# Kernel optimization log

Measured on AMD Instinct MI355X. Metric: run time of the kernel, lower is better.

## Reference

```python
import jax, jax.numpy as jnp
import numpy as np

TOP_K = 2
E = 8      # num_experts
D = 1024   # model dim
F = 2048   # expert hidden dim = int(2*3072/3), already a multiple of 256
B, S = 2, 1024


def setup_inputs() -> dict:
    key = jax.random.key(0)
    ks = jax.random.split(key, 8)
    sc = 0.02
    return {
        "x_bsD": jax.random.normal(ks[0], (B, S, D), dtype=jnp.float32),
        "router_DE": jax.random.normal(ks[1], (D, E), dtype=jnp.float32) * sc,
        "w_in_shared_FD": jax.random.normal(ks[2], (F, D), dtype=jnp.float32) * sc,
        "w_out_shared_DF": jax.random.normal(ks[3], (D, F), dtype=jnp.float32) * sc,
        "w_swiglu_FD": jax.random.normal(ks[4], (F, D), dtype=jnp.float32) * sc,
        "w_in_eDF": jax.random.normal(ks[5], (E, D, F), dtype=jnp.float32) * sc,
        "w_swiglu_eDF": jax.random.normal(ks[6], (E, D, F), dtype=jnp.float32) * sc,
        "w_out_eFD": jax.random.normal(ks[7], (E, F, D), dtype=jnp.float32) * sc,
    }


def reference(x_bsD, router_DE, w_in_shared_FD, w_out_shared_DF, w_swiglu_FD,
              w_in_eDF, w_swiglu_eDF, w_out_eFD):
    b, s, d = x_bsD.shape
    x_aD = x_bsD.reshape(-1, d)                      # [a, D]
    a = x_aD.shape[0]

    # Router (token choice): top-k per token, others masked to -inf
    scores_aE = x_aD @ router_DE                      # [a, E]
    topv_aK, topi_aK = jax.lax.top_k(scores_aE, TOP_K)
    masked_aE = jnp.full_like(scores_aE, -jnp.inf)
    masked_aE = masked_aE.at[jnp.arange(a)[:, None], topi_aK].set(topv_aK)
    # sigmoid(-inf) == 0 -> non-selected (expert, token) pairs contribute nothing
    gates_Ea = jax.nn.sigmoid(masked_aE.astype(jnp.float32)).astype(x_aD.dtype).T  # [E, a]

    # Dispatch: router_indices_EG == arange(a) per expert, so gather == broadcast
    routed_in_EaD = x_aD[None, :, :] * gates_Ea[:, :, None]   # [E, a, D]
    routed_in_EaD = jax.lax.stop_gradient(routed_in_EaD)      # matches .detach()

    # Per-expert bmm SwiGLU
    mid_EaF = jnp.einsum('ead,edf->eaf', routed_in_EaD, w_in_eDF)
    sw_EaF = jnp.einsum('ead,edf->eaf', routed_in_EaD, w_swiglu_eDF)
    h_EaF = jax.nn.silu(mid_EaF) * sw_EaF
    out_EaD = jnp.einsum('eaf,efd->ead', h_EaF, w_out_eFD)

    # Shared expert (computed under torch.no_grad in the original)
    shared_aF = jax.nn.silu(x_aD @ w_in_shared_FD.T) * (x_aD @ w_swiglu_FD.T)
    shared_out_aD = jax.lax.stop_gradient(shared_aF @ w_out_shared_DF.T)

    # Combine: scatter_add with per-expert arange indices == sum over experts
    out_aD = shared_out_aD + jnp.sum(out_EaD, axis=0)
    return out_aD.reshape(b, s, d)
```

## Files before the change

### kernel.cpp

```cpp
#include <hip/hip_runtime.h>
#include <hip/hip_bf16.h>

#define A_TOK 2048
#define DDIM 1024
#define FDIM 2048
#define NEXP 8
#define NE9 9
#define SLOTS_R (2 * A_TOK)
#define SLOTS_T (SLOTS_R + A_TOK)
#define NB1 (2 * FDIM)

typedef __attribute__((ext_vector_type(8))) short short8v;
typedef __attribute__((ext_vector_type(4))) float f32x4;
typedef __attribute__((ext_vector_type(4))) ushort ushort4v;

#define BARRIER() asm volatile("s_barrier" ::: "memory")
#define VMCNT(n) asm volatile("s_waitcnt vmcnt(" #n ")" ::: "memory")

__device__ __forceinline__ void lds16(const void* g, void* l) {
  __builtin_amdgcn_global_load_lds((const __attribute__((address_space(1))) void*)g,
                                   (__attribute__((address_space(3))) void*)l, 16, 0, 0);
}

__device__ __forceinline__ float sigmoidf_(float x) { return 1.f / (1.f + __expf(-x)); }
__device__ __forceinline__ ushort f2bf(float x) {
  __hip_bfloat16 b = __float2bfloat16(x);
  ushort u; __builtin_memcpy(&u, &b, 2); return u;
}
__device__ __forceinline__ float bf2f(ushort u) {
  union { unsigned int i; float f; } x; x.i = (unsigned int)u << 16; return x.f;
}

__global__ void k_trA(const float* __restrict__ w_in, const float* __restrict__ w_sw,
                      ushort* __restrict__ wt12) {
  int z = blockIdx.z; int e = z & 7; int which = z >> 3;
  const float* in = (which ? w_sw : w_in) + (size_t)e * DDIM * FDIM;
  ushort* outb = wt12 + (size_t)e * NB1 * DDIM;
  __shared__ ushort tile[64][68];
  int r0 = blockIdx.y * 64, c0 = blockIdx.x * 64;
  int tid = threadIdx.x;
  int rr = tid >> 4, cq = tid & 15;
#pragma unroll
  for (int i = 0; i < 4; i++) {
    int r = i * 16 + rr;
    float4 v = *(const float4*)(in + (size_t)(r0 + r) * FDIM + c0 + cq * 4);
    ushort4v o = {f2bf(v.x), f2bf(v.y), f2bf(v.z), f2bf(v.w)};
    *(ushort4v*)&tile[r][cq * 4] = o;
  }
  __syncthreads();
  int cc = tid >> 4, rq = tid & 15;
#pragma unroll
  for (int i = 0; i < 4; i++) {
    int c = i * 16 + cc;
    int f = c0 + c;
    int rp = ((f >> 5) << 6) + (which << 5) + (f & 31);
    ushort4v o = {tile[rq * 4 + 0][c], tile[rq * 4 + 1][c],
                  tile[rq * 4 + 2][c], tile[rq * 4 + 3][c]};
    *(ushort4v*)(outb + (size_t)rp * DDIM + r0 + rq * 4) = o;
  }
}

__global__ void k_trB(const float* __restrict__ in0, ushort* __restrict__ out0) {
  const float* in = in0 + (size_t)blockIdx.z * FDIM * DDIM;
  ushort* out = out0 + (size_t)blockIdx.z * DDIM * FDIM;
  __shared__ ushort tile[64][68];
  int r0 = blockIdx.y * 64, c0 = blockIdx.x * 64;
  int tid = threadIdx.x;
  int rr = tid >> 4, cq = tid & 15;
#pragma unroll
  for (int i = 0; i < 4; i++) {
    int r = i * 16 + rr;
    float4 v = *(const float4*)(in + (size_t)(r0 + r) * DDIM + c0 + cq * 4);
    ushort4v o = {f2bf(v.x), f2bf(v.y), f2bf(v.z), f2bf(v.w)};
    *(ushort4v*)&tile[r][cq * 4] = o;
  }
  __syncthreads();
  int cc = tid >> 4, rq = tid & 15;
#pragma unroll
  for (int i = 0; i < 4; i++) {
    int c = i * 16 + cc;
    ushort4v o = {tile[rq * 4 + 0][c], tile[rq * 4 + 1][c],
                  tile[rq * 4 + 2][c], tile[rq * 4 + 3][c]};
    *(ushort4v*)(out + (size_t)(c0 + c) * FDIM + r0 + rq * 4) = o;
  }
}

__global__ void k_cvt_sh(const float* __restrict__ w_in_sh, const float* __restrict__ w_sw_sh,
                         const float* __restrict__ w_out_sh, ushort* __restrict__ wt12_8,
                         ushort* __restrict__ wtout_8) {
  int z = blockIdx.y, row = blockIdx.x, tid = threadIdx.x;
  if (z < 2) {
    const float* in = (z ? w_sw_sh : w_in_sh) + (size_t)row * DDIM;
    int rp = ((row >> 5) << 6) + (z << 5) + (row & 31);
    ushort* outr = wt12_8 + (size_t)rp * DDIM;
    float4 v = ((const float4*)in)[tid];
    ushort4v o = {f2bf(v.x), f2bf(v.y), f2bf(v.z), f2bf(v.w)};
    ((ushort4v*)outr)[tid] = o;
  } else {
    if (row >= DDIM) return;
    const float* in = w_out_sh + (size_t)row * FDIM;
    ushort* outr = wtout_8 + (size_t)row * FDIM;
#pragma unroll
    for (int i = 0; i < 2; i++) {
      float4 v = ((const float4*)in)[tid + 256 * i];
      ushort4v o = {f2bf(v.x), f2bf(v.y), f2bf(v.z), f2bf(v.w)};
      ((ushort4v*)outr)[tid + 256 * i] = o;
    }
  }
}

__global__ void k_router(const float* __restrict__ x, const float* __restrict__ rw,
                         __hip_bfloat16* __restrict__ xbf, int* __restrict__ counts,
                         int* __restrict__ top_e, float* __restrict__ top_g) {
  int t = blockIdx.x * 4 + (threadIdx.x >> 6);
  int l = threadIdx.x & 63;
  const float* xr = x + (size_t)t * DDIM;
  float acc[NEXP];
#pragma unroll
  for (int e = 0; e < NEXP; e++) acc[e] = 0.f;
#pragma unroll
  for (int i = 0; i < 16; i++) {
    int d = i * 64 + l;
    float v = xr[d];
    xbf[(size_t)t * DDIM + d] = __float2bfloat16(v);
    const float* rr = rw + (size_t)d * NEXP;
#pragma unroll
    for (int e = 0; e < NEXP; e++) acc[e] += v * rr[e];
  }
#pragma unroll
  for (int e = 0; e < NEXP; e++) {
#pragma unroll
    for (int s = 32; s > 0; s >>= 1) acc[e] += __shfl_xor(acc[e], s);
  }
  if (l == 0) {
    float b1 = -1e30f, b2 = -1e30f;
    int i1 = 0, i2 = 0;
#pragma unroll
    for (int e = 0; e < NEXP; e++) {
      float v = acc[e];
      if (v > b1) { b2 = b1; i2 = i1; b1 = v; i1 = e; }
      else if (v > b2) { b2 = v; i2 = e; }
    }
    atomicAdd(&counts[i1], 1);
    atomicAdd(&counts[i2], 1);
    top_e[t * 2 + 0] = i1; top_e[t * 2 + 1] = i2;
    top_g[t * 2 + 0] = sigmoidf_(b1); top_g[t * 2 + 1] = sigmoidf_(b2);
  }
}

__global__ void k_scan(int* __restrict__ counts, int* __restrict__ offs,
                       int* __restrict__ cursor) {
  if (threadIdx.x == 0 && blockIdx.x == 0) {
    counts[NEXP] = A_TOK;
    int s = 0;
    for (int e = 0; e < NE9; e++) { offs[e] = s; s += counts[e]; cursor[e] = 0; }
  }
}

__global__ void k_dispatch(const float* __restrict__ x, const int* __restrict__ top_e,
                           const float* __restrict__ top_g, const int* __restrict__ offs,
                           int* __restrict__ cursor, int* __restrict__ slot_of,
                           __hip_bfloat16* __restrict__ y) {
  int t = blockIdx.x * 4 + (threadIdx.x >> 6);
  int l = threadIdx.x & 63;
  int e0 = top_e[t * 2 + 0], e1 = top_e[t * 2 + 1];
  float g0 = top_g[t * 2 + 0], g1 = top_g[t * 2 + 1];
  int s0 = 0, s1 = 0;
  if (l == 0) {
    s0 = offs[e0] + atomicAdd(&cursor[e0], 1);
    s1 = offs[e1] + atomicAdd(&cursor[e1], 1);
    slot_of[t * 2 + 0] = s0; slot_of[t * 2 + 1] = s1;
  }
  s0 = __shfl(s0, 0); s1 = __shfl(s1, 0);
  const float* xr = x + (size_t)t * DDIM;
#pragma unroll
  for (int i = 0; i < 16; i++) {
    int d = i * 64 + l;
    float v = xr[d];
    y[(size_t)s0 * DDIM + d] = __float2bfloat16(v * g0);
    y[(size_t)s1 * DDIM + d] = __float2bfloat16(v * g1);
  }
}

__global__ __launch_bounds__(256, 3) void k_mlp1(
    const ushort* __restrict__ Abase, const ushort* __restrict__ Bbase,
    ushort* __restrict__ Obase, const int* __restrict__ d_cnt,
    const int* __restrict__ d_off) {
  constexpr int K = DDIM, NT = DDIM / 32;
  constexpr int BUF = 16384;
  __shared__ __align__(16) char smem[3 * BUF];
  int e = blockIdx.z;
  int cnt = d_cnt[e];
  int m0 = blockIdx.y * 128;
  if (m0 >= cnt) return;
  int roff = d_off[e];
  int n0 = blockIdx.x * 128;
  const ushort* B = Bbase + (size_t)e * NB1 * DDIM;
  int tid = threadIdx.x, w = tid >> 6, l = tid & 63;
  int wm = w >> 1, wn = w & 1, lr = l & 15, kg = l >> 4;
  size_t arow0 = (size_t)roff + m0;

  int srow = tid >> 2;
  int sgg = (tid & 3) ^ ((tid >> 3) & 3);
  const ushort* pA0 = Abase + (arow0 + srow) * (size_t)K + sgg * 8;
  const ushort* pA1 = pA0 + (size_t)64 * K;
  const ushort* pB0 = B + ((size_t)n0 + srow) * K + sgg * 8;
  const ushort* pB1 = pB0 + (size_t)64 * K;
  int tls = tid * 16;

  int xorg = (kg ^ ((lr >> 1) & 3)) << 4;
  int offA[4], offB[4];
#pragma unroll
  for (int i = 0; i < 4; i++) {
    offA[i] = (wm * 64 + i * 16 + lr) * 64 + xorg;
    offB[i] = 8192 + (wn * 64 + i * 16 + lr) * 64 + xorg;
  }

  f32x4 acc[4][4];
#pragma unroll
  for (int i = 0; i < 4; i++)
#pragma unroll
    for (int j = 0; j < 4; j++) acc[i][j] = {0.f, 0.f, 0.f, 0.f};

#pragma unroll
  for (int pt = 0; pt < 2; ++pt) {
    char* bb = smem + pt * BUF;
    lds16(pA0, bb + tls);         pA0 += 32;
    lds16(pA1, bb + 4096 + tls);  pA1 += 32;
    lds16(pB0, bb + 8192 + tls);  pB0 += 32;
    lds16(pB1, bb + 12288 + tls); pB1 += 32;
  }
  VMCNT(4);
  BARRIER();

  char* b0 = smem;
  char* b1 = smem + BUF;
  char* b2 = smem + 2 * BUF;
  for (int t = 0; t < NT; ++t) {
    bool st = (t + 2) < NT;
    short8v af[4], bf[4];
#pragma unroll
    for (int mf = 0; mf < 4; mf++) af[mf] = *(const short8v*)(b0 + offA[mf]);
#pragma unroll
    for (int nf = 0; nf < 2; nf++) bf[nf] = *(const short8v*)(b0 + offB[nf]);
    if (st) {
      lds16(pA0, b2 + tls);
      lds16(pA1, b2 + 4096 + tls);
    }
    pA0 += 32; pA1 += 32;
    BARRIER();
    __builtin_amdgcn_s_setprio(1);
#pragma unroll
    for (int nf = 0; nf < 2; nf++)
#pragma unroll
      for (int mf = 0; mf < 4; mf++)
        acc[mf][nf] = __builtin_amdgcn_mfma_f32_16x16x32_bf16(af[mf], bf[nf], acc[mf][nf], 0, 0, 0);
    __builtin_amdgcn_s_setprio(0);
    BARRIER();
#pragma unroll
    for (int nf = 2; nf < 4; nf++) bf[nf] = *(const short8v*)(b0 + offB[nf]);
    if (st) {
      lds16(pB0, b2 + 8192 + tls);
      lds16(pB1, b2 + 12288 + tls);
    }
    pB0 += 32; pB1 += 32;
    BARRIER();
    __builtin_amdgcn_s_setprio(1);
#pragma unroll
    for (int nf = 2; nf < 4; nf++)
#pragma unroll
      for (int mf = 0; mf < 4; mf++)
        acc[mf][nf] = __builtin_amdgcn_mfma_f32_16x16x32_bf16(af[mf], bf[nf], acc[mf][nf], 0, 0, 0);
    __builtin_amdgcn_s_setprio(0);
    if (t < NT - 1) {
      if (st) { VMCNT(4); } else { VMCNT(0); }
      BARRIER();
    }
    char* tmp = b0; b0 = b1; b1 = b2; b2 = tmp;
  }

  int j = (n0 >> 6) + wn;
#pragma unroll
  for (int mf = 0; mf < 4; mf++)
#pragma unroll
    for (int nf = 0; nf < 2; nf++)
#pragma unroll
      for (int r = 0; r < 4; r++) {
        int row = m0 + wm * 64 + mf * 16 + kg * 4 + r;
        if (row < cnt) {
          float mid = acc[mf][nf][r];
          float sw = acc[mf][nf + 2][r];
          float hv = mid * sigmoidf_(mid) * sw;
          int col = j * 32 + nf * 16 + lr;
          Obase[((size_t)roff + row) * FDIM + col] = f2bf(hv);
        }
      }
}

__global__ __launch_bounds__(256, 3) void k_mlp2(
    const ushort* __restrict__ Abase, const ushort* __restrict__ Bbase,
    ushort* __restrict__ part, const int* __restrict__ d_cnt,
    const int* __restrict__ d_off) {
  constexpr int K = FDIM, NT = 1024 / 32;
  constexpr int BUF = 16384;
  __shared__ __align__(16) char smem[3 * BUF];
  int e = blockIdx.z;
  int cnt = d_cnt[e];
  int mt = blockIdx.y >> 1, kz = blockIdx.y & 1;
  int m0 = mt * 128;
  if (m0 >= cnt) return;
  int roff = d_off[e];
  int n0 = blockIdx.x * 128;
  int kbeg = kz * 1024;
  const ushort* B = Bbase + (size_t)e * DDIM * FDIM;
  int tid = threadIdx.x, w = tid >> 6, l = tid & 63;
  int wm = w >> 1, wn = w & 1, lr = l & 15, kg = l >> 4;
  size_t arow0 = (size_t)roff + m0;

  int srow = tid >> 2;
  int sgg = (tid & 3) ^ ((tid >> 3) & 3);
  const ushort* pA0 = Abase + (arow0 + srow) * (size_t)K + kbeg + sgg * 8;
  const ushort* pA1 = pA0 + (size_t)64 * K;
  const ushort* pB0 = B + ((size_t)n0 + srow) * K + kbeg + sgg * 8;
  const ushort* pB1 = pB0 + (size_t)64 * K;
  int tls = tid * 16;

  int xorg = (kg ^ ((lr >> 1) & 3)) << 4;
  int offA[4], offB[4];
#pragma unroll
  for (int i = 0; i < 4; i++) {
    offA[i] = (wm * 64 + i * 16 + lr) * 64 + xorg;
    offB[i] = 8192 + (wn * 64 + i * 16 + lr) * 64 + xorg;
  }

  f32x4 acc[4][4];
#pragma unroll
  for (int i = 0; i < 4; i++)
#pragma unroll
    for (int j = 0; j < 4; j++) acc[i][j] = {0.f, 0.f, 0.f, 0.f};

#pragma unroll
  for (int pt = 0; pt < 2; ++pt) {
    char* bb = smem + pt * BUF;
    lds16(pA0, bb + tls);         pA0 += 32;
    lds16(pA1, bb + 4096 + tls);  pA1 += 32;
    lds16(pB0, bb + 8192 + tls);  pB0 += 32;
    lds16(pB1, bb + 12288 + tls); pB1 += 32;
  }
  VMCNT(4);
  BARRIER();

  char* b0 = smem;
  char* b1 = smem + BUF;
  char* b2 = smem + 2 * BUF;
  for (int t = 0; t < NT; ++t) {
    bool st = (t + 2) < NT;
    short8v af[4], bf[4];
#pragma unroll
    for (int mf = 0; mf < 4; mf++) af[mf] = *(const short8v*)(b0 + offA[mf]);
#pragma unroll
    for (int nf = 0; nf < 2; nf++) bf[nf] = *(const short8v*)(b0 + offB[nf]);
    if (st) {
      lds16(pA0, b2 + tls);
      lds16(pA1, b2 + 4096 + tls);
    }
    pA0 += 32; pA1 += 32;
    BARRIER();
    __builtin_amdgcn_s_setprio(1);
#pragma unroll
    for (int nf = 0; nf < 2; nf++)
#pragma unroll
      for (int mf = 0; mf < 4; mf++)
        acc[mf][nf] = __builtin_amdgcn_mfma_f32_16x16x32_bf16(af[mf], bf[nf], acc[mf][nf], 0, 0, 0);
    __builtin_amdgcn_s_setprio(0);
    BARRIER();
#pragma unroll
    for (int nf = 2; nf < 4; nf++) bf[nf] = *(const short8v*)(b0 + offB[nf]);
    if (st) {
      lds16(pB0, b2 + 8192 + tls);
      lds16(pB1, b2 + 12288 + tls);
    }
    pB0 += 32; pB1 += 32;
    BARRIER();
    __builtin_amdgcn_s_setprio(1);
#pragma unroll
    for (int nf = 2; nf < 4; nf++)
#pragma unroll
      for (int mf = 0; mf < 4; mf++)
        acc[mf][nf] = __builtin_amdgcn_mfma_f32_16x16x32_bf16(af[mf], bf[nf], acc[mf][nf], 0, 0, 0);
    __builtin_amdgcn_s_setprio(0);
    if (t < NT - 1) {
      if (st) { VMCNT(4); } else { VMCNT(0); }
      BARRIER();
    }
    char* tmp = b0; b0 = b1; b1 = b2; b2 = tmp;
  }

  ushort* outp = part + (size_t)kz * SLOTS_T * DDIM;
#pragma unroll
  for (int mf = 0; mf < 4; mf++)
#pragma unroll
    for (int nf = 0; nf < 4; nf++)
#pragma unroll
      for (int r = 0; r < 4; r++) {
        int row = m0 + wm * 64 + mf * 16 + kg * 4 + r;
        if (row < cnt) {
          int col = n0 + wn * 64 + nf * 16 + lr;
          outp[((size_t)roff + row) * DDIM + col] = f2bf(acc[mf][nf][r]);
        }
      }
}

__global__ void k_combine(const ushort* __restrict__ part, const int* __restrict__ slot_of,
                          float* __restrict__ out) {
  int t = blockIdx.x, q = threadIdx.x;
  int rows[3];
  rows[0] = slot_of[t * 2 + 0];
  rows[1] = slot_of[t * 2 + 1];
  rows[2] = SLOTS_R + t;
  size_t P = (size_t)SLOTS_T * DDIM;
  float o[4] = {0.f, 0.f, 0.f, 0.f};
#pragma unroll
  for (int kz = 0; kz < 2; kz++)
#pragma unroll
    for (int i = 0; i < 3; i++) {
      ushort4v v = *(const ushort4v*)(part + kz * P + (size_t)rows[i] * DDIM + q * 4);
#pragma unroll
      for (int j = 0; j < 4; j++) o[j] += bf2f(v[j]);
    }
  float4 ov = {o[0], o[1], o[2], o[3]};
  ((float4*)out)[(size_t)t * (DDIM / 4) + q] = ov;
}

extern "C" void kernel_launch(void* const* d_in, const int* in_sizes, int n_in,
                              void* d_out, int out_size, void* d_ws, size_t ws_size,
                              hipStream_t stream) {
  (void)in_sizes; (void)n_in; (void)out_size; (void)ws_size;
  const float* x        = (const float*)d_in[0];
  const float* router   = (const float*)d_in[1];
  const float* w_in_sh  = (const float*)d_in[2];
  const float* w_out_sh = (const float*)d_in[3];
  const float* w_sw_sh  = (const float*)d_in[4];
  const float* w_in_e   = (const float*)d_in[5];
  const float* w_sw_e   = (const float*)d_in[6];
  const float* w_out_e  = (const float*)d_in[7];
  float* out = (float*)d_out;

  char* ws = (char*)d_ws;
  size_t off = 0;
  auto alloc = [&](size_t bytes) -> char* {
    char* p = ws + off;
    off += (bytes + 255) & ~(size_t)255;
    return p;
  };
  ushort* wt12     = (ushort*)alloc((size_t)NE9 * NB1 * DDIM * 2);
  ushort* wt_out_t = (ushort*)alloc((size_t)NE9 * DDIM * FDIM * 2);
  __hip_bfloat16* y_all = (__hip_bfloat16*)alloc((size_t)SLOTS_R * DDIM * 2);
  __hip_bfloat16* xbf   = (__hip_bfloat16*)alloc((size_t)A_TOK * DDIM * 2);
  ushort* h        = (ushort*)alloc((size_t)SLOTS_T * FDIM * 2);
  int*   counts  = (int*)alloc(64);
  int*   offs    = (int*)alloc(64);
  int*   cursor  = (int*)alloc(64);
  int*   top_e   = (int*)alloc((size_t)A_TOK * 2 * 4);
  float* top_g   = (float*)alloc((size_t)A_TOK * 2 * 4);
  int*   slot_of = (int*)alloc((size_t)A_TOK * 2 * 4);
  (void)alloc(1 << 20);
  ushort* part = wt12;

  hipMemsetAsync(counts, 0, 64, stream);

  k_trA<<<dim3(FDIM / 64, DDIM / 64, 16), 256, 0, stream>>>(w_in_e, w_sw_e, wt12);
  k_trB<<<dim3(DDIM / 64, FDIM / 64, NEXP), 256, 0, stream>>>(w_out_e, wt_out_t);
  k_cvt_sh<<<dim3(FDIM, 3), 256, 0, stream>>>(
      w_in_sh, w_sw_sh, w_out_sh,
      wt12 + (size_t)NEXP * NB1 * DDIM, wt_out_t + (size_t)NEXP * DDIM * FDIM);

  k_router<<<dim3(A_TOK / 4), 256, 0, stream>>>(x, router, xbf, counts, top_e, top_g);
  k_scan<<<1, 64, 0, stream>>>(counts, offs, cursor);
  k_dispatch<<<dim3(A_TOK / 4), 256, 0, stream>>>(x, top_e, top_g, offs, cursor, slot_of, y_all);

  k_mlp1<<<dim3(NB1 / 128, A_TOK / 128, NE9), 256, 0, stream>>>(
      (const ushort*)y_all, wt12, h, counts, offs);

  k_mlp2<<<dim3(DDIM / 128, (A_TOK / 128) * 2, NE9), 256, 0, stream>>>(
      h, wt_out_t, part, counts, offs);

  k_combine<<<dim3(A_TOK), 256, 0, stream>>>(part, slot_of, out);
}
```

Before: 305.0 us.

## Fuse weight-prep kernels, fold scan into router, remap GEMM grids across XCDs

Merges the three weight conversion/transposition kernels and the counts memset into a single prep kernel, and folds the expert-offset scan into the router with a last-block ticket. This removes several kernel launches and a memset. The MLP GEMM grids are flattened to 1D and remapped so consecutive workgroups, which land on different XCDs, are spread across experts and tiles. That remap is meant to improve L2 locality and load balance. The ticket pattern relies on threadfence ordering for correctness.

```diff
diff --git a/kernel.cpp b/kernel.cpp
--- a/kernel.cpp
+++ b/kernel.cpp
@@ -10,6 +10,12 @@
 #define SLOTS_T (SLOTS_R + A_TOK)
 #define NB1 (2 * FDIM)
 
+#define PREP_TRA_END 8192
+#define PREP_TRB_END (PREP_TRA_END + 4096)
+#define PREP_SH12_END (PREP_TRB_END + 1024)
+#define PREP_SHOUT_END (PREP_SH12_END + 512)
+#define PREP_NWG (PREP_SHOUT_END + 1)
+
 typedef __attribute__((ext_vector_type(8))) short short8v;
 typedef __attribute__((ext_vector_type(4))) float f32x4;
 typedef __attribute__((ext_vector_type(4))) ushort ushort4v;
@@ -31,87 +37,100 @@
   union { unsigned int i; float f; } x; x.i = (unsigned int)u << 16; return x.f;
 }
 
-__global__ void k_trA(const float* __restrict__ w_in, const float* __restrict__ w_sw,
-                      ushort* __restrict__ wt12) {
-  int z = blockIdx.z; int e = z & 7; int which = z >> 3;
-  const float* in = (which ? w_sw : w_in) + (size_t)e * DDIM * FDIM;
-  ushort* outb = wt12 + (size_t)e * NB1 * DDIM;
+__global__ void k_prep(const float* __restrict__ w_in_e, const float* __restrict__ w_sw_e,
+                       const float* __restrict__ w_out_e, const float* __restrict__ w_in_sh,
+                       const float* __restrict__ w_sw_sh, const float* __restrict__ w_out_sh,
+                       ushort* __restrict__ wt12, ushort* __restrict__ wt_out_t,
+                       int* __restrict__ counts, int* __restrict__ ticket) {
   __shared__ ushort tile[64][68];
-  int r0 = blockIdx.y * 64, c0 = blockIdx.x * 64;
-  int tid = threadIdx.x;
-  int rr = tid >> 4, cq = tid & 15;
-#pragma unroll
-  for (int i = 0; i < 4; i++) {
-    int r = i * 16 + rr;
-    float4 v = *(const float4*)(in + (size_t)(r0 + r) * FDIM + c0 + cq * 4);
-    ushort4v o = {f2bf(v.x), f2bf(v.y), f2bf(v.z), f2bf(v.w)};
-    *(ushort4v*)&tile[r][cq * 4] = o;
-  }
-  __syncthreads();
-  int cc = tid >> 4, rq = tid & 15;
-#pragma unroll
-  for (int i = 0; i < 4; i++) {
-    int c = i * 16 + cc;
-    int f = c0 + c;
+  int b = blockIdx.x, tid = threadIdx.x;
+  if (b < PREP_TRA_END) {
+    int z = b >> 9, t2 = b & 511;
+    int e = z & 7, which = z >> 3;
+    const float* in = (which ? w_sw_e : w_in_e) + (size_t)e * DDIM * FDIM;
+    ushort* outb = wt12 + (size_t)e * NB1 * DDIM;
+    int c0 = (t2 & 31) * 64, r0 = (t2 >> 5) * 64;
+    int rr = tid >> 4, cq = tid & 15;
+#pragma unroll
+    for (int i = 0; i < 4; i++) {
+      int r = i * 16 + rr;
+      float4 v = *(const float4*)(in + (size_t)(r0 + r) * FDIM + c0 + cq * 4);
+      ushort4v o = {f2bf(v.x), f2bf(v.y), f2bf(v.z), f2bf(v.w)};
+      *(ushort4v*)&tile[r][cq * 4] = o;
+    }
+    __syncthreads();
+    int cc = tid >> 4, rq = tid & 15;
+#pragma unroll
+    for (int i = 0; i < 4; i++) {
+      int c = i * 16 + cc;
+      int f = c0 + c;
+      int rp = ((f >> 5) << 6) + (which << 5) + (f & 31);
+      ushort4v o = {tile[rq * 4 + 0][c], tile[rq * 4 + 1][c],
+                    tile[rq * 4 + 2][c], tile[rq * 4 + 3][c]};
+      *(ushort4v*)(outb + (size_t)rp * DDIM + r0 + rq * 4) = o;
+    }
+  } else if (b < PREP_TRB_END) {
+    int b2 = b - PREP_TRA_END;
+    int z = b2 >> 9, t2 = b2 & 511;
+    const float* in = w_out_e + (size_t)z * FDIM * DDIM;
+    ushort* out = wt_out_t + (size_t)z * DDIM * FDIM;
+    int c0 = (t2 & 15) * 64, r0 = (t2 >> 4) * 64;
+    int rr = tid >> 4, cq = tid & 15;
+#pragma unroll
+    for (int i = 0; i < 4; i++) {
+      int r = i * 16 + rr;
+      float4 v = *(const float4*)(in + (size_t)(r0 + r) * DDIM + c0 + cq * 4);
+      ushort4v o = {f2bf(v.x), f2bf(v.y), f2bf(v.z), f2bf(v.w)};
+      *(ushort4v*)&tile[r][cq * 4] = o;
+    }
+    __syncthreads();
+    int cc = tid >> 4, rq = tid & 15;
+#pragma unroll
+    for (int i = 0; i < 4; i++) {
+      int c = i * 16 + cc;
+      ushort4v o = {tile[rq * 4 + 0][c], tile[rq * 4 + 1][c],
+                    tile[rq * 4 + 2][c], tile[rq * 4 + 3][c]};
+      *(ushort4v*)(out + (size_t)(c0 + c) * FDIM + r0 + rq * 4) = o;
+    }
+  } else if (b < PREP_SH12_END) {
+    int j = b - PREP_TRB_END;
+    int rj = j * 4 + (tid >> 6);
+    int l = tid & 63;
+    int which = rj & 1, f = rj >> 1;
+    const float* src = (which ? w_sw_sh : w_in_sh) + (size_t)f * DDIM;
     int rp = ((f >> 5) << 6) + (which << 5) + (f & 31);
-    ushort4v o = {tile[rq * 4 + 0][c], tile[rq * 4 + 1][c],
-                  tile[rq * 4 + 2][c], tile[rq * 4 + 3][c]};
-    *(ushort4v*)(outb + (size_t)rp * DDIM + r0 + rq * 4) = o;
-  }
-}
-
-__global__ void k_trB(const float* __restrict__ in0, ushort* __restrict__ out0) {
-  const float* in = in0 + (size_t)blockIdx.z * FDIM * DDIM;
-  ushort* out = out0 + (size_t)blockIdx.z * DDIM * FDIM;
-  __shared__ ushort tile[64][68];
-  int r0 = blockIdx.y * 64, c0 = blockIdx.x * 64;
-  int tid = threadIdx.x;
-  int rr = tid >> 4, cq = tid & 15;
-#pragma unroll
-  for (int i = 0; i < 4; i++) {
-    int r = i * 16 + rr;
-    float4 v = *(const float4*)(in + (size_t)(r0 + r) * DDIM + c0 + cq * 4);
-    ushort4v o = {f2bf(v.x), f2bf(v.y), f2bf(v.z), f2bf(v.w)};
-    *(ushort4v*)&tile[r][cq * 4] = o;
-  }
-  __syncthreads();
-  int cc = tid >> 4, rq = tid & 15;
-#pragma unroll
-  for (int i = 0; i < 4; i++) {
-    int c = i * 16 + cc;
-    ushort4v o = {tile[rq * 4 + 0][c], tile[rq * 4 + 1][c],
-                  tile[rq * 4 + 2][c], tile[rq * 4 + 3][c]};
-    *(ushort4v*)(out + (size_t)(c0 + c) * FDIM + r0 + rq * 4) = o;
-  }
-}
-
-__global__ void k_cvt_sh(const float* __restrict__ w_in_sh, const float* __restrict__ w_sw_sh,
-                         const float* __restrict__ w_out_sh, ushort* __restrict__ wt12_8,
-                         ushort* __restrict__ wtout_8) {
-  int z = blockIdx.y, row = blockIdx.x, tid = threadIdx.x;
-  if (z < 2) {
-    const float* in = (z ? w_sw_sh : w_in_sh) + (size_t)row * DDIM;
-    int rp = ((row >> 5) << 6) + (z << 5) + (row & 31);
-    ushort* outr = wt12_8 + (size_t)rp * DDIM;
-    float4 v = ((const float4*)in)[tid];
-    ushort4v o = {f2bf(v.x), f2bf(v.y), f2bf(v.z), f2bf(v.w)};
-    ((ushort4v*)outr)[tid] = o;
+    ushort* dst = wt12 + (size_t)NEXP * NB1 * DDIM + (size_t)rp * DDIM;
+#pragma unroll
+    for (int i = 0; i < 4; i++) {
+      int q = l + 64 * i;
+      float4 v = ((const float4*)src)[q];
+      ushort4v o = {f2bf(v.x), f2bf(v.y), f2bf(v.z), f2bf(v.w)};
+      ((ushort4v*)dst)[q] = o;
+    }
+  } else if (b < PREP_SHOUT_END) {
+    int j = b - PREP_SH12_END;
+    int d = j * 2 + (tid >> 7);
+    int l = tid & 127;
+    const float* src = w_out_sh + (size_t)d * FDIM;
+    ushort* dst = wt_out_t + (size_t)NEXP * DDIM * FDIM + (size_t)d * FDIM;
+#pragma unroll
+    for (int i = 0; i < 4; i++) {
+      int q = l + 128 * i;
+      float4 v = ((const float4*)src)[q];
+      ushort4v o = {f2bf(v.x), f2bf(v.y), f2bf(v.z), f2bf(v.w)};
+      ((ushort4v*)dst)[q] = o;
+    }
   } else {
-    if (row >= DDIM) return;
-    const float* in = w_out_sh + (size_t)row * FDIM;
-    ushort* outr = wtout_8 + (size_t)row * FDIM;
-#pragma unroll
-    for (int i = 0; i < 2; i++) {
-      float4 v = ((const float4*)in)[tid + 256 * i];
-      ushort4v o = {f2bf(v.x), f2bf(v.y), f2bf(v.z), f2bf(v.w)};
-      ((ushort4v*)outr)[tid + 256 * i] = o;
-    }
+    if (tid < 16) counts[tid] = 0;
+    if (tid == 16) *ticket = 0;
   }
 }
 
 __global__ void k_router(const float* __restrict__ x, const float* __restrict__ rw,
                          __hip_bfloat16* __restrict__ xbf, int* __restrict__ counts,
-                         int* __restrict__ top_e, float* __restrict__ top_g) {
+                         int* __restrict__ top_e, float* __restrict__ top_g,
+                         int* __restrict__ offs, int* __restrict__ cursor,
+                         int* __restrict__ ticket) {
   int t = blockIdx.x * 4 + (threadIdx.x >> 6);
   int l = threadIdx.x & 63;
   const float* xr = x + (size_t)t * DDIM;
@@ -146,14 +165,16 @@
     top_e[t * 2 + 0] = i1; top_e[t * 2 + 1] = i2;
     top_g[t * 2 + 0] = sigmoidf_(b1); top_g[t * 2 + 1] = sigmoidf_(b2);
   }
-}
-
-__global__ void k_scan(int* __restrict__ counts, int* __restrict__ offs,
-                       int* __restrict__ cursor) {
-  if (threadIdx.x == 0 && blockIdx.x == 0) {
-    counts[NEXP] = A_TOK;
-    int s = 0;
-    for (int e = 0; e < NE9; e++) { offs[e] = s; s += counts[e]; cursor[e] = 0; }
+  __syncthreads();
+  if (threadIdx.x == 0) {
+    __threadfence();
+    int tk = atomicAdd(ticket, 1);
+    if (tk == gridDim.x - 1) {
+      counts[NEXP] = A_TOK;
+      int s = 0;
+      for (int e = 0; e < NE9; e++) { offs[e] = s; s += counts[e]; cursor[e] = 0; }
+      __threadfence();
+    }
   }
 }
 
@@ -189,12 +210,15 @@
   constexpr int K = DDIM, NT = DDIM / 32;
   constexpr int BUF = 16384;
   __shared__ __align__(16) char smem[3 * BUF];
-  int e = blockIdx.z;
+  int bid = blockIdx.x;
+  int L = (bid & 7) * 576 + (bid >> 3);
+  int e = L / 512;
+  int rem = L - e * 512;
   int cnt = d_cnt[e];
-  int m0 = blockIdx.y * 128;
+  int m0 = (rem & 15) * 128;
   if (m0 >= cnt) return;
   int roff = d_off[e];
-  int n0 = blockIdx.x * 128;
+  int n0 = (rem >> 4) * 128;
   const ushort* B = Bbase + (size_t)e * NB1 * DDIM;
   int tid = threadIdx.x, w = tid >> 6, l = tid & 63;
   int wm = w >> 1, wn = w & 1, lr = l & 15, kg = l >> 4;
@@ -304,13 +328,17 @@
   constexpr int K = FDIM, NT = 1024 / 32;
   constexpr int BUF = 16384;
   __shared__ __align__(16) char smem[3 * BUF];
-  int e = blockIdx.z;
+  int bid = blockIdx.x;
+  int L = (bid & 7) * 288 + (bid >> 3);
+  int e = L / 256;
+  int rem = L - e * 256;
   int cnt = d_cnt[e];
-  int mt = blockIdx.y >> 1, kz = blockIdx.y & 1;
+  int sub = rem & 31;
+  int mt = sub >> 1, kz = sub & 1;
   int m0 = mt * 128;
   if (m0 >= cnt) return;
   int roff = d_off[e];
-  int n0 = blockIdx.x * 128;
+  int n0 = (rem >> 5) * 128;
   int kbeg = kz * 1024;
   const ushort* B = Bbase + (size_t)e * DDIM * FDIM;
   int tid = threadIdx.x, w = tid >> 6, l = tid & 63;
@@ -461,28 +489,26 @@
   int*   counts  = (int*)alloc(64);
   int*   offs    = (int*)alloc(64);
   int*   cursor  = (int*)alloc(64);
+  int*   ticket  = (int*)alloc(64);
   int*   top_e   = (int*)alloc((size_t)A_TOK * 2 * 4);
   float* top_g   = (float*)alloc((size_t)A_TOK * 2 * 4);
   int*   slot_of = (int*)alloc((size_t)A_TOK * 2 * 4);
   (void)alloc(1 << 20);
   ushort* part = wt12;
 
-  hipMemsetAsync(counts, 0, 64, stream);
-
-  k_trA<<<dim3(FDIM / 64, DDIM / 64, 16), 256, 0, stream>>>(w_in_e, w_sw_e, wt12);
-  k_trB<<<dim3(DDIM / 64, FDIM / 64, NEXP), 256, 0, stream>>>(w_out_e, wt_out_t);
-  k_cvt_sh<<<dim3(FDIM, 3), 256, 0, stream>>>(
-      w_in_sh, w_sw_sh, w_out_sh,
-      wt12 + (size_t)NEXP * NB1 * DDIM, wt_out_t + (size_t)NEXP * DDIM * FDIM);
-
-  k_router<<<dim3(A_TOK / 4), 256, 0, stream>>>(x, router, xbf, counts, top_e, top_g);
-  k_scan<<<1, 64, 0, stream>>>(counts, offs, cursor);
+  k_prep<<<dim3(PREP_NWG), 256, 0, stream>>>(
+      w_in_e, w_sw_e, w_out_e, w_in_sh, w_sw_sh, w_out_sh,
+      wt12, wt_out_t, counts, ticket);
+
+  k_router<<<dim3(A_TOK / 4), 256, 0, stream>>>(x, router, xbf, counts, top_e, top_g,
+                                                offs, cursor, ticket);
+
   k_dispatch<<<dim3(A_TOK / 4), 256, 0, stream>>>(x, top_e, top_g, offs, cursor, slot_of, y_all);
 
-  k_mlp1<<<dim3(NB1 / 128, A_TOK / 128, NE9), 256, 0, stream>>>(
+  k_mlp1<<<dim3(32 * 16 * NE9), 256, 0, stream>>>(
       (const ushort*)y_all, wt12, h, counts, offs);
 
-  k_mlp2<<<dim3(DDIM / 128, (A_TOK / 128) * 2, NE9), 256, 0, stream>>>(
+  k_mlp2<<<dim3(8 * 32 * NE9), 256, 0, stream>>>(
       h, wt_out_t, part, counts, offs);
 
   k_combine<<<dim3(A_TOK), 256, 0, stream>>>(part, slot_of, out);
```

Result: slower. 408.5 us (+33.9%).

## Fuse fp32-to-bf16 weight conversion and transpose into expert GEMM B-tile loads

Applied to the files above, without the earlier changes.

Drops the separate weight transpose and conversion kernels. Both GEMMs now read the fp32 weights straight from global memory into registers, pack them to bf16 with the needed transpose, and write them into swizzled LDS. The main loop also moves from a three-stage async pipeline to a double buffer with register staging. This avoids writing and re-reading about 150 MB of bf16 weight copies, but each output tile now reads fp32 weights again, the weights are converted redundantly across M tiles, and vmcnt(0) waits each iteration weaken load/compute overlap.

```diff
diff --git a/kernel.cpp b/kernel.cpp
--- a/kernel.cpp
+++ b/kernel.cpp
@@ -15,7 +15,8 @@
 typedef __attribute__((ext_vector_type(4))) ushort ushort4v;
 
 #define BARRIER() asm volatile("s_barrier" ::: "memory")
-#define VMCNT(n) asm volatile("s_waitcnt vmcnt(" #n ")" ::: "memory")
+#define VMCNT0() asm volatile("s_waitcnt vmcnt(0)" ::: "memory")
+#define LGKM0() asm volatile("s_waitcnt lgkmcnt(0)" ::: "memory")
 
 __device__ __forceinline__ void lds16(const void* g, void* l) {
   __builtin_amdgcn_global_load_lds((const __attribute__((address_space(1))) void*)g,
@@ -30,83 +31,8 @@
 __device__ __forceinline__ float bf2f(ushort u) {
   union { unsigned int i; float f; } x; x.i = (unsigned int)u << 16; return x.f;
 }
-
-__global__ void k_trA(const float* __restrict__ w_in, const float* __restrict__ w_sw,
-                      ushort* __restrict__ wt12) {
-  int z = blockIdx.z; int e = z & 7; int which = z >> 3;
-  const float* in = (which ? w_sw : w_in) + (size_t)e * DDIM * FDIM;
-  ushort* outb = wt12 + (size_t)e * NB1 * DDIM;
-  __shared__ ushort tile[64][68];
-  int r0 = blockIdx.y * 64, c0 = blockIdx.x * 64;
-  int tid = threadIdx.x;
-  int rr = tid >> 4, cq = tid & 15;
-#pragma unroll
-  for (int i = 0; i < 4; i++) {
-    int r = i * 16 + rr;
-    float4 v = *(const float4*)(in + (size_t)(r0 + r) * FDIM + c0 + cq * 4);
-    ushort4v o = {f2bf(v.x), f2bf(v.y), f2bf(v.z), f2bf(v.w)};
-    *(ushort4v*)&tile[r][cq * 4] = o;
-  }
-  __syncthreads();
-  int cc = tid >> 4, rq = tid & 15;
-#pragma unroll
-  for (int i = 0; i < 4; i++) {
-    int c = i * 16 + cc;
-    int f = c0 + c;
-    int rp = ((f >> 5) << 6) + (which << 5) + (f & 31);
-    ushort4v o = {tile[rq * 4 + 0][c], tile[rq * 4 + 1][c],
-                  tile[rq * 4 + 2][c], tile[rq * 4 + 3][c]};
-    *(ushort4v*)(outb + (size_t)rp * DDIM + r0 + rq * 4) = o;
-  }
-}
-
-__global__ void k_trB(const float* __restrict__ in0, ushort* __restrict__ out0) {
-  const float* in = in0 + (size_t)blockIdx.z * FDIM * DDIM;
-  ushort* out = out0 + (size_t)blockIdx.z * DDIM * FDIM;
-  __shared__ ushort tile[64][68];
-  int r0 = blockIdx.y * 64, c0 = blockIdx.x * 64;
-  int tid = threadIdx.x;
-  int rr = tid >> 4, cq = tid & 15;
-#pragma unroll
-  for (int i = 0; i < 4; i++) {
-    int r = i * 16 + rr;
-    float4 v = *(const float4*)(in + (size_t)(r0 + r) * DDIM + c0 + cq * 4);
-    ushort4v o = {f2bf(v.x), f2bf(v.y), f2bf(v.z), f2bf(v.w)};
-    *(ushort4v*)&tile[r][cq * 4] = o;
-  }
-  __syncthreads();
-  int cc = tid >> 4, rq = tid & 15;
-#pragma unroll
-  for (int i = 0; i < 4; i++) {
-    int c = i * 16 + cc;
-    ushort4v o = {tile[rq * 4 + 0][c], tile[rq * 4 + 1][c],
-                  tile[rq * 4 + 2][c], tile[rq * 4 + 3][c]};
-    *(ushort4v*)(out + (size_t)(c0 + c) * FDIM + r0 + rq * 4) = o;
-  }
-}
-
-__global__ void k_cvt_sh(const float* __restrict__ w_in_sh, const float* __restrict__ w_sw_sh,
-                         const float* __restrict__ w_out_sh, ushort* __restrict__ wt12_8,
-                         ushort* __restrict__ wtout_8) {
-  int z = blockIdx.y, row = blockIdx.x, tid = threadIdx.x;
-  if (z < 2) {
-    const float* in = (z ? w_sw_sh : w_in_sh) + (size_t)row * DDIM;
-    int rp = ((row >> 5) << 6) + (z << 5) + (row & 31);
-    ushort* outr = wt12_8 + (size_t)rp * DDIM;
-    float4 v = ((const float4*)in)[tid];
-    ushort4v o = {f2bf(v.x), f2bf(v.y), f2bf(v.z), f2bf(v.w)};
-    ((ushort4v*)outr)[tid] = o;
-  } else {
-    if (row >= DDIM) return;
-    const float* in = w_out_sh + (size_t)row * FDIM;
-    ushort* outr = wtout_8 + (size_t)row * FDIM;
-#pragma unroll
-    for (int i = 0; i < 2; i++) {
-      float4 v = ((const float4*)in)[tid + 256 * i];
-      ushort4v o = {f2bf(v.x), f2bf(v.y), f2bf(v.z), f2bf(v.w)};
-      ((ushort4v*)outr)[tid + 256 * i] = o;
-    }
-  }
+__device__ __forceinline__ unsigned pk2(float a, float b) {
+  return (unsigned)f2bf(a) | ((unsigned)f2bf(b) << 16);
 }
 
 __global__ void k_router(const float* __restrict__ x, const float* __restrict__ rw,
@@ -183,37 +109,60 @@
 }
 
 __global__ __launch_bounds__(256, 3) void k_mlp1(
-    const ushort* __restrict__ Abase, const ushort* __restrict__ Bbase,
-    ushort* __restrict__ Obase, const int* __restrict__ d_cnt,
-    const int* __restrict__ d_off) {
-  constexpr int K = DDIM, NT = DDIM / 32;
-  constexpr int BUF = 16384;
-  __shared__ __align__(16) char smem[3 * BUF];
+    const ushort* __restrict__ Abase, const float* __restrict__ w_in_e,
+    const float* __restrict__ w_sw_e, const float* __restrict__ w_in_sh,
+    const float* __restrict__ w_sw_sh, ushort* __restrict__ Obase,
+    const int* __restrict__ d_cnt, const int* __restrict__ d_off) {
+  constexpr int NT = 32;
+  __shared__ __align__(16) char smem[32768];
   int e = blockIdx.z;
   int cnt = d_cnt[e];
   int m0 = blockIdx.y * 128;
   if (m0 >= cnt) return;
   int roff = d_off[e];
-  int n0 = blockIdx.x * 128;
-  const ushort* B = Bbase + (size_t)e * NB1 * DDIM;
+  int n0b = blockIdx.x * 128;
   int tid = threadIdx.x, w = tid >> 6, l = tid & 63;
   int wm = w >> 1, wn = w & 1, lr = l & 15, kg = l >> 4;
   size_t arow0 = (size_t)roff + m0;
 
   int srow = tid >> 2;
   int sgg = (tid & 3) ^ ((tid >> 3) & 3);
-  const ushort* pA0 = Abase + (arow0 + srow) * (size_t)K + sgg * 8;
-  const ushort* pA1 = pA0 + (size_t)64 * K;
-  const ushort* pB0 = B + ((size_t)n0 + srow) * K + sgg * 8;
-  const ushort* pB1 = pB0 + (size_t)64 * K;
+  const ushort* pA0 = Abase + (arow0 + srow) * (size_t)DDIM + sgg * 8;
+  const ushort* pA1 = pA0 + (size_t)64 * DDIM;
   int tls = tid * 16;
+
+  int kq = tid >> 5, nq = tid & 31;
+  int nl0 = nq * 4;
+  int nprime = n0b + nl0;
+  int which = (nprime >> 5) & 1;
+  bool shared_e = (e == NEXP);
+  const float* pB;
+  size_t bst;
+  int badv;
+  if (!shared_e) {
+    int f0 = ((nprime >> 6) << 5) + (nprime & 31);
+    const float* wb = which ? w_sw_e : w_in_e;
+    pB = wb + (size_t)e * DDIM * FDIM + (size_t)(kq * 4) * FDIM + f0;
+    bst = FDIM; badv = 32 * FDIM;
+  } else {
+    int f0 = ((nprime >> 6) << 5) + (nprime & 31);
+    const float* wb = which ? w_sw_sh : w_in_sh;
+    pB = wb + (size_t)f0 * DDIM + kq * 4;
+    bst = DDIM; badv = 32;
+  }
+  int wofs[4];
+#pragma unroll
+  for (int j = 0; j < 4; j++) {
+    int nloc = nl0 + j;
+    wofs[j] = nloc * 64 + ((((kq >> 1) ^ ((nloc >> 1) & 3)) << 4) | ((kq & 1) << 3));
+  }
 
   int xorg = (kg ^ ((lr >> 1) & 3)) << 4;
   int offA[4], offB[4];
 #pragma unroll
   for (int i = 0; i < 4; i++) {
     offA[i] = (wm * 64 + i * 16 + lr) * 64 + xorg;
-    offB[i] = 8192 + (wn * 64 + i * 16 + lr) * 64 + xorg;
+    offB[i] = (wn * 64 + i * 16 + lr) * 64 + xorg;
   }
 
   f32x4 acc[4][4];
@@ -222,64 +171,78 @@
 #pragma unroll
     for (int j = 0; j < 4; j++) acc[i][j] = {0.f, 0.f, 0.f, 0.f};
 
-#pragma unroll
-  for (int pt = 0; pt < 2; ++pt) {
-    char* bb = smem + pt * BUF;
-    lds16(pA0, bb + tls);         pA0 += 32;
-    lds16(pA1, bb + 4096 + tls);  pA1 += 32;
-    lds16(pB0, bb + 8192 + tls);  pB0 += 32;
-    lds16(pB1, bb + 12288 + tls); pB1 += 32;
-  }
-  VMCNT(4);
+  char* bufA0 = smem;
+  char* bufA1 = smem + 8192;
+  char* bufB0 = smem + 16384;
+  char* bufB1 = smem + 24576;
+
+  float4 rb0, rb1, rb2, rb3;
+  auto loadB = [&]() {
+    rb0 = *(const float4*)(pB);
+    rb1 = *(const float4*)(pB + bst);
+    rb2 = *(const float4*)(pB + 2 * bst);
+    rb3 = *(const float4*)(pB + 3 * bst);
+    pB += badv;
+  };
+  auto writeB = [&](char* bb) {
+    uint2 w0, w1, w2, w3;
+    if (!shared_e) {
+      w0 = {pk2(rb0.x, rb1.x), pk2(rb2.x, rb3.x)};
+      w1 = {pk2(rb0.y, rb1.y), pk2(rb2.y, rb3.y)};
+      w2 = {pk2(rb0.z, rb1.z), pk2(rb2.z, rb3.z)};
+      w3 = {pk2(rb0.w, rb1.w), pk2(rb2.w, rb3.w)};
+    } else {
+      w0 = {pk2(rb0.x, rb0.y), pk2(rb0.z, rb0.w)};
+      w1 = {pk2(rb1.x, rb1.y), pk2(rb1.z, rb1.w)};
+      w2 = {pk2(rb2.x, rb2.y), pk2(rb2.z, rb2.w)};
+      w3 = {pk2(rb3.x, rb3.y), pk2(rb3.z, rb3.w)};
+    }
+    *(uint2*)(bb + wofs[0]) = w0;
+    *(uint2*)(bb + wofs[1]) = w1;
+    *(uint2*)(bb + wofs[2]) = w2;
+    *(uint2*)(bb + wofs[3]) = w3;
+  };
+
+  loadB();
+  lds16(pA0, bufA0 + tls); lds16(pA1, bufA0 + 4096 + tls);
+  pA0 += 32; pA1 += 32;
+  VMCNT0();
+  writeB(bufB0);
+  LGKM0();
   BARRIER();
 
-  char* b0 = smem;
-  char* b1 = smem + BUF;
-  char* b2 = smem + 2 * BUF;
+  char* cA = bufA0; char* nA = bufA1;
+  char* cB = bufB0; char* nB = bufB1;
   for (int t = 0; t < NT; ++t) {
-    bool st = (t + 2) < NT;
+    bool stg = (t + 1) < NT;
+    if (stg) {
+      loadB();
+      lds16(pA0, nA + tls); lds16(pA1, nA + 4096 + tls);
+      pA0 += 32; pA1 += 32;
+    }
     short8v af[4], bf[4];
 #pragma unroll
-    for (int mf = 0; mf < 4; mf++) af[mf] = *(const short8v*)(b0 + offA[mf]);
-#pragma unroll
-    for (int nf = 0; nf < 2; nf++) bf[nf] = *(const short8v*)(b0 + offB[nf]);
-    if (st) {
-      lds16(pA0, b2 + tls);
-      lds16(pA1, b2 + 4096 + tls);
-    }
-    pA0 += 32; pA1 += 32;
-    BARRIER();
+    for (int i = 0; i < 4; i++) af[i] = *(const short8v*)(cA + offA[i]);
+#pragma unroll
+    for (int i = 0; i < 4; i++) bf[i] = *(const short8v*)(cB + offB[i]);
     __builtin_amdgcn_s_setprio(1);
 #pragma unroll
-    for (int nf = 0; nf < 2; nf++)
+    for (int nf = 0; nf < 4; nf++)
 #pragma unroll
       for (int mf = 0; mf < 4; mf++)
         acc[mf][nf] = __builtin_amdgcn_mfma_f32_16x16x32_bf16(af[mf], bf[nf], acc[mf][nf], 0, 0, 0);
     __builtin_amdgcn_s_setprio(0);
-    BARRIER();
-#pragma unroll
-    for (int nf = 2; nf < 4; nf++) bf[nf] = *(const short8v*)(b0 + offB[nf]);
-    if (st) {
-      lds16(pB0, b2 + 8192 + tls);
-      lds16(pB1, b2 + 12288 + tls);
-    }
-    pB0 += 32; pB1 += 32;
-    BARRIER();
-    __builtin_amdgcn_s_setprio(1);
-#pragma unroll
-    for (int nf = 2; nf < 4; nf++)
-#pragma unroll
-      for (int mf = 0; mf < 4; mf++)
-        acc[mf][nf] = __builtin_amdgcn_mfma_f32_16x16x32_bf16(af[mf], bf[nf], acc[mf][nf], 0, 0, 0);
-    __builtin_amdgcn_s_setprio(0);
-    if (t < NT - 1) {
-      if (st) { VMCNT(4); } else { VMCNT(0); }
+    if (stg) {
+      VMCNT0();
+      writeB(nB);
+      LGKM0();
       BARRIER();
-    }
-    char* tmp = b0; b0 = b1; b1 = b2; b2 = tmp;
-  }
-
-  int j = (n0 >> 6) + wn;
+      char* tp = cA; cA = nA; nA = tp;
+      tp = cB; cB = nB; nB = tp;
+    }
+  }
+
+  int j = (n0b >> 6) + wn;
 #pragma unroll
   for (int mf = 0; mf < 4; mf++)
 #pragma unroll
@@ -298,39 +261,56 @@
 }
 
 __global__ __launch_bounds__(256, 3) void k_mlp2(
-    const ushort* __restrict__ Abase, const ushort* __restrict__ Bbase,
-    ushort* __restrict__ part, const int* __restrict__ d_cnt,
-    const int* __restrict__ d_off) {
-  constexpr int K = FDIM, NT = 1024 / 32;
-  constexpr int BUF = 16384;
-  __shared__ __align__(16) char smem[3 * BUF];
+    const ushort* __restrict__ Abase, const float* __restrict__ w_out_e,
+    const float* __restrict__ w_out_sh, ushort* __restrict__ part,
+    const int* __restrict__ d_cnt, const int* __restrict__ d_off) {
+  constexpr int NT = 32;
+  __shared__ __align__(16) char smem[32768];
   int e = blockIdx.z;
   int cnt = d_cnt[e];
   int mt = blockIdx.y >> 1, kz = blockIdx.y & 1;
   int m0 = mt * 128;
   if (m0 >= cnt) return;
   int roff = d_off[e];
-  int n0 = blockIdx.x * 128;
+  int n0b = blockIdx.x * 128;
   int kbeg = kz * 1024;
-  const ushort* B = Bbase + (size_t)e * DDIM * FDIM;
   int tid = threadIdx.x, w = tid >> 6, l = tid & 63;
   int wm = w >> 1, wn = w & 1, lr = l & 15, kg = l >> 4;
   size_t arow0 = (size_t)roff + m0;
 
   int srow = tid >> 2;
   int sgg = (tid & 3) ^ ((tid >> 3) & 3);
-  const ushort* pA0 = Abase + (arow0 + srow) * (size_t)K + kbeg + sgg * 8;
-  const ushort* pA1 = pA0 + (size_t)64 * K;
-  const ushort* pB0 = B + ((size_t)n0 + srow) * K + kbeg + sgg * 8;
-  const ushort* pB1 = pB0 + (size_t)64 * K;
+  const ushort* pA0 = Abase + (arow0 + srow) * (size_t)FDIM + kbeg + sgg * 8;
+  const ushort* pA1 = pA0 + (size_t)64 * FDIM;
   int tls = tid * 16;
+
+  int kq = tid >> 5, nq = tid & 31;
+  int nl0 = nq * 4;
+  int nprime = n0b + nl0;
+  bool shared_e = (e == NEXP);
+  const float* pB;
+  size_t bst;
+  int badv;
+  if (!shared_e) {
+    pB = w_out_e + (size_t)e * FDIM * DDIM + (size_t)(kbeg + kq * 4) * DDIM + nprime;
+    bst = DDIM; badv = 32 * DDIM;
+  } else {
+    pB = w_out_sh + (size_t)nprime * FDIM + kbeg + kq * 4;
+    bst = FDIM; badv = 32;
+  }
+  int wofs[4];
+#pragma unroll
+  for (int j = 0; j < 4; j++) {
+    int nloc = nl0 + j;
+    wofs[j] = nloc * 64 + ((((kq >> 1) ^ ((nloc >> 1) & 3)) << 4) | ((kq & 1) << 3));
+  }
 
   int xorg = (kg ^ ((lr >> 1) & 3)) << 4;
   int offA[4], offB[4];
 #pragma unroll
   for (int i = 0; i < 4; i++) {
     offA[i] = (wm * 64 + i * 16 + lr) * 64 + xorg;
-    offB[i] = 8192 + (wn * 64 + i * 16 + lr) * 64 + xorg;
+    offB[i] = (wn * 64 + i * 16 + lr) * 64 + xorg;
   }
 
   f32x4 acc[4][4];
@@ -339,61 +319,75 @@
 #pragma unroll
     for (int j = 0; j < 4; j++) acc[i][j] = {0.f, 0.f, 0.f, 0.f};
 
-#pragma unroll
-  for (int pt = 0; pt < 2; ++pt) {
-    char* bb = smem + pt * BUF;
-    lds16(pA0, bb + tls);         pA0 += 32;
-    lds16(pA1, bb + 4096 + tls);  pA1 += 32;
-    lds16(pB0, bb + 8192 + tls);  pB0 += 32;
-    lds16(pB1, bb + 12288 + tls); pB1 += 32;
-  }
-  VMCNT(4);
+  char* bufA0 = smem;
+  char* bufA1 = smem + 8192;
+  char* bufB0 = smem + 16384;
+  char* bufB1 = smem + 24576;
+
+  float4 rb0, rb1, rb2, rb3;
+  auto loadB = [&]() {
+    rb0 = *(const float4*)(pB);
+    rb1 = *(const float4*)(pB + bst);
+    rb2 = *(const float4*)(pB + 2 * bst);
+    rb3 = *(const float4*)(pB + 3 * bst);
+    pB += badv;
+  };
+  auto writeB = [&](char* bb) {
+    uint2 w0, w1, w2, w3;
+    if (!shared_e) {
+      w0 = {pk2(rb0.x, rb1.x), pk2(rb2.x, rb3.x)};
+      w1 = {pk2(rb0.y, rb1.y), pk2(rb2.y, rb3.y)};
+      w2 = {pk2(rb0.z, rb1.z), pk2(rb2.z, rb3.z)};
+      w3 = {pk2(rb0.w, rb1.w), pk2(rb2.w, rb3.w)};
+    } else {
+      w0 = {pk2(rb0.x, rb0.y), pk2(rb0.z, rb0.w)};
+      w1 = {pk2(rb1.x, rb1.y), pk2(rb1.z, rb1.w)};
+      w2 = {pk2(rb2.x, rb2.y), pk2(rb2.z, rb2.w)};
+      w3 = {pk2(rb3.x, rb3.y), pk2(rb3.z, rb3.w)};
+    }
+    *(uint2*)(bb + wofs[0]) = w0;
+    *(uint2*)(bb + wofs[1]) = w1;
+    *(uint2*)(bb + wofs[2]) = w2;
+    *(uint2*)(bb + wofs[3]) = w3;
+  };
+
+  loadB();
+  lds16(pA0, bufA0 + tls); lds16(pA1, bufA0 + 4096 + tls);
+  pA0 += 32; pA1 += 32;
+  VMCNT0();
+  writeB(bufB0);
+  LGKM0();
   BARRIER();
 
-  char* b0 = smem;
-  char* b1 = smem + BUF;
-  char* b2 = smem + 2 * BUF;
+  char* cA = bufA0; char* nA = bufA1;
+  char* cB = bufB0; char* nB = bufB1;
   for (int t = 0; t < NT; ++t) {
-    bool st = (t + 2) < NT;
+    bool stg = (t + 1) < NT;
+    if (stg) {
+      loadB();
+      lds16(pA0, nA + tls); lds16(pA1, nA + 4096 + tls);
+      pA0 += 32; pA1 += 32;
+    }
     short8v af[4], bf[4];
 #pragma unroll
-    for (int mf = 0; mf < 4; mf++) af[mf] = *(const short8v*)(b0 + offA[mf]);
-#pragma unroll
-    for (int nf = 0; nf < 2; nf++) bf[nf] = *(const short8v*)(b0 + offB[nf]);
-    if (st) {
-      lds16(pA0, b2 + tls);
-      lds16(pA1, b2 + 4096 + tls);
-    }
-    pA0 += 32; pA1 += 32;
-    BARRIER();
+    for (int i = 0; i < 4; i++) af[i] = *(const short8v*)(cA + offA[i]);
+#pragma unroll
+    for (int i = 0; i < 4; i++) bf[i] = *(const short8v*)(cB + offB[i]);
     __builtin_amdgcn_s_setprio(1);
 #pragma unroll
-    for (int nf = 0; nf < 2; nf++)
+    for (int nf = 0; nf < 4; nf++)
 #pragma unroll
       for (int mf = 0; mf < 4; mf++)
         acc[mf][nf] = __builtin_amdgcn_mfma_f32_16x16x32_bf16(af[mf], bf[nf], acc[mf][nf], 0, 0, 0);
     __builtin_amdgcn_s_setprio(0);
-    BARRIER();
-#pragma unroll
-    for (int nf = 2; nf < 4; nf++) bf[nf] = *(const short8v*)(b0 + offB[nf]);
-    if (st) {
-      lds16(pB0, b2 + 8192 + tls);
-      lds16(pB1, b2 + 12288 + tls);
-    }
-    pB0 += 32; pB1 += 32;
-    BARRIER();
-    __builtin_amdgcn_s_setprio(1);
-#pragma unroll
-    for (int nf = 2; nf < 4; nf++)
-#pragma unroll
-      for (int mf = 0; mf < 4; mf++)
-        acc[mf][nf] = __builtin_amdgcn_mfma_f32_16x16x32_bf16(af[mf], bf[nf], acc[mf][nf], 0, 0, 0);
-    __builtin_amdgcn_s_setprio(0);
-    if (t < NT - 1) {
-      if (st) { VMCNT(4); } else { VMCNT(0); }
+    if (stg) {
+      VMCNT0();
+      writeB(nB);
+      LGKM0();
       BARRIER();
-    }
-    char* tmp = b0; b0 = b1; b1 = b2; b2 = tmp;
+      char* tp = cA; cA = nA; nA = tp;
+      tp = cB; cB = nB; nB = tp;
+    }
   }
 
   ushort* outp = part + (size_t)kz * SLOTS_T * DDIM;
@@ -405,7 +399,7 @@
       for (int r = 0; r < 4; r++) {
         int row = m0 + wm * 64 + mf * 16 + kg * 4 + r;
         if (row < cnt) {
-          int col = n0 + wn * 64 + nf * 16 + lr;
+          int col = n0b + wn * 64 + nf * 16 + lr;
           outp[((size_t)roff + row) * DDIM + col] = f2bf(acc[mf][nf][r]);
         }
       }
@@ -453,11 +447,10 @@
     off += (bytes + 255) & ~(size_t)255;
     return p;
   };
-  ushort* wt12     = (ushort*)alloc((size_t)NE9 * NB1 * DDIM * 2);
-  ushort* wt_out_t = (ushort*)alloc((size_t)NE9 * DDIM * FDIM * 2);
   __hip_bfloat16* y_all = (__hip_bfloat16*)alloc((size_t)SLOTS_R * DDIM * 2);
   __hip_bfloat16* xbf   = (__hip_bfloat16*)alloc((size_t)A_TOK * DDIM * 2);
-  ushort* h        = (ushort*)alloc((size_t)SLOTS_T * FDIM * 2);
+  ushort* h    = (ushort*)alloc((size_t)SLOTS_T * FDIM * 2);
+  ushort* part = (ushort*)alloc((size_t)2 * SLOTS_T * DDIM * 2);
   int*   counts  = (int*)alloc(64);
   int*   offs    = (int*)alloc(64);
   int*   cursor  = (int*)alloc(64);
@@ -465,25 +458,18 @@
   float* top_g   = (float*)alloc((size_t)A_TOK * 2 * 4);
   int*   slot_of = (int*)alloc((size_t)A_TOK * 2 * 4);
   (void)alloc(1 << 20);
-  ushort* part = wt12;
 
   hipMemsetAsync(counts, 0, 64, stream);
-
-  k_trA<<<dim3(FDIM / 64, DDIM / 64, 16), 256, 0, stream>>>(w_in_e, w_sw_e, wt12);
-  k_trB<<<dim3(DDIM / 64, FDIM / 64, NEXP), 256, 0, stream>>>(w_out_e, wt_out_t);
-  k_cvt_sh<<<dim3(FDIM, 3), 256, 0, stream>>>(
-      w_in_sh, w_sw_sh, w_out_sh,
-      wt12 + (size_t)NEXP * NB1 * DDIM, wt_out_t + (size_t)NEXP * DDIM * FDIM);
 
   k_router<<<dim3(A_TOK / 4), 256, 0, stream>>>(x, router, xbf, counts, top_e, top_g);
   k_scan<<<1, 64, 0, stream>>>(counts, offs, cursor);
   k_dispatch<<<dim3(A_TOK / 4), 256, 0, stream>>>(x, top_e, top_g, offs, cursor, slot_of, y_all);
 
   k_mlp1<<<dim3(NB1 / 128, A_TOK / 128, NE9), 256, 0, stream>>>(
-      (const ushort*)y_all, wt12, h, counts, offs);
+      (const ushort*)y_all, w_in_e, w_sw_e, w_in_sh, w_sw_sh, h, counts, offs);
 
   k_mlp2<<<dim3(DDIM / 128, (A_TOK / 128) * 2, NE9), 256, 0, stream>>>(
-      h, wt_out_t, part, counts, offs);
+      h, w_out_e, w_out_sh, part, counts, offs);
 
   k_combine<<<dim3(A_TOK), 256, 0, stream>>>(part, slot_of, out);
 }
```

Result: no change. 310.7 us (+1.9%).
